# Kernel tuning notes

Measured on AMD Instinct MI355X. Metric: run time of the kernel, lower is better.

Reference implementation:

```python
import jax, jax.numpy as jnp
import numpy as np

HIDDEN = 2560
HEADS = 32
HEAD_DIM = HIDDEN // HEADS  # 80
ROT = HEAD_DIM // 2         # partial_rotary_factor=0.5 -> 40
B = 2
S = 2048
T = B * S
THETA = 10000.0


def setup_inputs() -> dict:
    key = jax.random.key(0)
    k0, k1, k2, k3, k4 = jax.random.split(key, 5)
    hidden_states = jax.random.normal(k0, (T, HIDDEN), jnp.float32)
    w_qkv = jax.random.normal(k1, (3 * HIDDEN, HIDDEN), jnp.float32) * 0.02
    b_qkv = jax.random.normal(k2, (3 * HIDDEN,), jnp.float32) * 0.02
    w_o = jax.random.normal(k3, (HIDDEN, HIDDEN), jnp.float32) * 0.02
    b_o = jax.random.normal(k4, (HIDDEN,), jnp.float32) * 0.02
    # rotary tables for positions 0..S-1 per sequence, rotary_dim=ROT
    pos = jnp.tile(jnp.arange(S, dtype=jnp.float32), B)  # [T]
    inv_freq = 1.0 / (THETA ** (jnp.arange(0, ROT, 2, dtype=jnp.float32) / ROT))  # [ROT//2]
    freqs = pos[:, None] * inv_freq[None, :]  # [T, ROT//2]
    return {
        "hidden_states": hidden_states,
        "w_qkv": w_qkv,
        "b_qkv": b_qkv,
        "w_o": w_o,
        "b_o": b_o,
        "cos": jnp.cos(freqs),
        "sin": jnp.sin(freqs),
        "batch": B,
    }


def _apply_rope(x, cos, sin):
    # x: [T, H, D]; rotate first ROT dims NeoX-style (rotate_half)
    half = ROT // 2
    x1 = x[..., :half]
    x2 = x[..., half:ROT]
    c = cos[:, None, :]
    s = sin[:, None, :]
    return jnp.concatenate([x1 * c - x2 * s, x1 * s + x2 * c, x[..., ROT:]], axis=-1)


def reference(hidden_states, w_qkv, b_qkv, w_o, b_o, cos, sin, batch):
    t, hdim = hidden_states.shape
    seq = t // batch
    # fused QKV projection (with bias)
    qkv = hidden_states @ w_qkv.T + b_qkv  # [T, 3*HIDDEN]
    q, k, v = jnp.split(qkv, 3, axis=1)
    q = _apply_rope(q.reshape(t, HEADS, HEAD_DIM), cos, sin)
    k = _apply_rope(k.reshape(t, HEADS, HEAD_DIM), cos, sin)
    v = v.reshape(t, HEADS, HEAD_DIM)
    # prefill causal attention per sequence
    qb = q.reshape(batch, seq, HEADS, HEAD_DIM)
    kb = k.reshape(batch, seq, HEADS, HEAD_DIM)
    vb = v.reshape(batch, seq, HEADS, HEAD_DIM)
    scale = 1.0 / jnp.sqrt(jnp.float32(HEAD_DIM))
    scores = jnp.einsum("bqhd,bkhd->bhqk", qb, kb) * scale  # [B,H,S,S]
    causal = jnp.tril(jnp.ones((seq, seq), dtype=bool))
    scores = jnp.where(causal[None, None], scores, jnp.finfo(scores.dtype).min)
    attn = jax.nn.softmax(scores, axis=-1)
    out = jnp.einsum("bhqk,bkhd->bqhd", attn, vb).reshape(t, HIDDEN)
    return out @ w_o.T + b_o
```

## Files before the change

### kernel.cpp

```cpp
#include <hip/hip_runtime.h>
#include <hip/hip_bf16.h>

#define HID   2560
#define NH    32
#define HD    80
#define SEQ   2048
#define TTOT  4096
#define QKVN  7680

typedef float  f32x4  __attribute__((ext_vector_type(4)));
typedef short  short8 __attribute__((ext_vector_type(8)));
typedef __bf16 bf16x8 __attribute__((ext_vector_type(8)));
typedef __hip_bfloat16 bf16;

__device__ __forceinline__ float bf2f(bf16 h) { return __bfloat162float(h); }
__device__ __forceinline__ bf16  f2bf(float f) { return __float2bfloat16(f); }

__device__ __forceinline__ f32x4 mfma16(short8 a, short8 b, f32x4 c) {
  return __builtin_amdgcn_mfma_f32_16x16x32_bf16(
      __builtin_bit_cast(bf16x8, a), __builtin_bit_cast(bf16x8, b), c, 0, 0, 0);
}

typedef __attribute__((address_space(1))) const unsigned int as1_uint;
typedef __attribute__((address_space(3))) unsigned int       as3_uint;
__device__ __forceinline__ void gld16(const void* g, void* l) {
  __builtin_amdgcn_global_load_lds((as1_uint*)g, (as3_uint*)l, 16, 0, 0);
}

__global__ void detect_kernel(const unsigned short* __restrict__ hid, int* flag) {
  const int tid = threadIdx.x;
  const unsigned short u = hid[2 * (tid * 997)];
  const int e = (u >> 7) & 0xFF;
  const int sane = (u == 0 || (e >= 0x60 && e <= 0x8A)) ? 1 : 0;
  __shared__ int cnt;
  if (tid == 0) cnt = 0;
  __syncthreads();
  atomicAdd(&cnt, sane);
  __syncthreads();
  if (tid == 0) *flag = (cnt < 160) ? 1 : 0;
}

__global__ void convert_kernel(const void* __restrict__ src, bf16* __restrict__ dst,
                               int n8, const int* __restrict__ flag) {
  const bool isf32 = (*flag != 0);
  for (int i = blockIdx.x * 256 + threadIdx.x; i < n8; i += gridDim.x * 256) {
    if (isf32) {
      const float4* s = (const float4*)src;
      float4 a = s[2 * i], b = s[2 * i + 1];
      __align__(16) bf16 o8[8] = {f2bf(a.x), f2bf(a.y), f2bf(a.z), f2bf(a.w),
                                  f2bf(b.x), f2bf(b.y), f2bf(b.z), f2bf(b.w)};
      *(uint4*)(dst + 8 * i) = *(const uint4*)o8;
    } else {
      *(uint4*)(dst + 8 * i) = ((const uint4*)src)[i];
    }
  }
}

__global__ void emit_kernel(const bf16* __restrict__ src, void* __restrict__ dst,
                            int n8, const int* __restrict__ flag) {
  const bool isf32 = (*flag != 0);
  for (int i = blockIdx.x * 256 + threadIdx.x; i < n8; i += gridDim.x * 256) {
    uint4 v = *(const uint4*)(src + 8 * i);
    if (isf32) {
      const bf16* b = (const bf16*)&v;
      float4* d = (float4*)dst;
      d[2 * i]     = make_float4(bf2f(b[0]), bf2f(b[1]), bf2f(b[2]), bf2f(b[3]));
      d[2 * i + 1] = make_float4(bf2f(b[4]), bf2f(b[5]), bf2f(b[6]), bf2f(b[7]));
    } else {
      ((uint4*)dst)[i] = v;
    }
  }
}

__global__ __launch_bounds__(512, 2) void gemm256_bias(
    const bf16* __restrict__ A, const bf16* __restrict__ B,
    const bf16* __restrict__ bias, bf16* __restrict__ C,
    int M, int N, int K)
{
  __shared__ __align__(16) bf16 lA[3][16384];
  __shared__ __align__(16) bf16 lB[2][16384];

  const int tid  = threadIdx.x;
  const int wid  = tid >> 6;
  const int lane = tid & 63;
  const int quad = lane >> 4;
  const int l15  = lane & 15;
  const int wr   = wid >> 2;
  const int wc   = wid & 3;

  int wgid;
  {
    const int nwg = gridDim.x;
    const int q = nwg >> 3, r = nwg & 7;
    const int xcd = blockIdx.x & 7, lin = blockIdx.x >> 3;
    wgid = (xcd < r ? xcd * (q + 1) : r * (q + 1) + (xcd - r) * q) + lin;
  }
  const int gx = M >> 8;
  const int m0 = (wgid % gx) << 8;
  const int n0 = (wgid / gx) << 8;

  const int NT = K >> 6;

  const int rr   = tid >> 3;
  const int cbyt = ((tid & 7) << 4) ^ ((rr & 7) << 4);
  const size_t o1 = (size_t)rr * K + (cbyt >> 1);
  const size_t o2 = o1 + (size_t)64 * K;

  const bf16* Ab = A + (size_t)m0 * K;
  const bf16* Bb = B + (size_t)n0 * K;

#define STAGEA(bufsel, half, tt)                                               \
  {                                                                            \
    const bf16* _s = Ab + (size_t)(half) * 128 * K + (size_t)(tt) * 64;        \
    bf16* _d = &lA[bufsel][(half) * 8192 + wid * 512];                         \
    gld16(_s + o1, _d);                                                        \
    gld16(_s + o2, _d + 4096);                                                 \
  }
#define STAGEB(bufsel, half, tt)                                               \
  {                                                                            \
    const bf16* _s = Bb + (size_t)(half) * 128 * K + (size_t)(tt) * 64;        \
    bf16* _d = &lB[bufsel][(half) * 8192 + wid * 512];                         \
    gld16(_s + o1, _d);                                                        \
    gld16(_s + o2, _d + 4096);                                                 \
  }

#define WAIT_LGKM0                                                             \
  do {                                                                         \
    asm volatile("s_waitcnt lgkmcnt(0)" ::: "memory");                         \
    __builtin_amdgcn_sched_barrier(0);                                         \
  } while (0)
#define WAIT_VM(n) asm volatile("s_waitcnt vmcnt(" #n ")" ::: "memory")

  const int csw0 = ((quad ^ (l15 & 7)) << 4);
  const int csw1 = (((4 | quad) ^ (l15 & 7)) << 4);

  f32x4 acc[8][4];
#pragma unroll
  for (int i = 0; i < 8; ++i)
#pragma unroll
    for (int j = 0; j < 4; ++j) acc[i][j] = (f32x4)0.f;

  short8 a[4][2], b23[2][2], b01A[2][2], b01B[2][2];

  STAGEA(0, 0, 0); STAGEA(0, 1, 0);
  STAGEB(0, 0, 0); STAGEB(0, 1, 0);
  if (NT > 1) {
    STAGEA(1, 0, 1); STAGEA(1, 1, 1);
    STAGEB(1, 0, 1); STAGEB(1, 1, 1);
    WAIT_VM(8);
  } else {
    WAIT_VM(0);
  }
  __builtin_amdgcn_s_barrier();
#pragma unroll
  for (int n = 0; n < 2; ++n) {
    const char* p = (const char*)lB[0] + (size_t)(wc * 64 + n * 16 + l15) * 128;
    b01A[n][0] = *(const short8*)(p + csw0);
    b01A[n][1] = *(const short8*)(p + csw1);
  }

#define KTILE(T, B01U, B01L)                                                   \
  do {                                                                         \
    const int _t = (T);                                                        \
    const bf16* Al = lA[_t % 3];                                               \
    const bf16* Bl = lB[_t & 1];                                               \
    const bf16* Bln = lB[(_t + 1) & 1];                                        \
    const bool stg = (_t + 2 < NT);                                            \
    const bool nxt = (_t + 1 < NT);                                            \
             \
    _Pragma("unroll") for (int mi = 0; mi < 4; ++mi) {                         \
      const char* p = (const char*)Al + (size_t)(wr * 128 + mi * 16 + l15) * 128; \
      a[mi][0] = *(const short8*)(p + csw0);                                   \
      a[mi][1] = *(const short8*)(p + csw1);                                   \
    }                                                                          \
    if (stg) STAGEA((_t + 2) % 3, 0, _t + 2);                                  \
    WAIT_LGKM0;                                                                \
    __builtin_amdgcn_s_setprio(1);                                             \
    _Pragma("unroll") for (int mi = 0; mi < 4; ++mi)                           \
      _Pragma("unroll") for (int n = 0; n < 2; ++n) {                          \
        acc[mi][n] = mfma16(a[mi][0], B01U[n][0], acc[mi][n]);                 \
        acc[mi][n] = mfma16(a[mi][1], B01U[n][1], acc[mi][n]);                 \
      }                                                                        \
    __builtin_amdgcn_s_setprio(0);                                             \
                \
    _Pragma("unroll") for (int n = 0; n < 2; ++n) {                            \
      const char* p = (const char*)Bl + (size_t)(wc * 64 + (2 + n) * 16 + l15) * 128; \
      b23[n][0] = *(const short8*)(p + csw0);                                  \
      b23[n][1] = *(const short8*)(p + csw1);                                  \
    }                                                                          \
    if (stg) STAGEA((_t + 2) % 3, 1, _t + 2);                                  \
    WAIT_LGKM0;                                                                \
    __builtin_amdgcn_s_setprio(1);                                             \
    _Pragma("unroll") for (int mi = 0; mi < 4; ++mi)                           \
      _Pragma("unroll") for (int n = 0; n < 2; ++n) {                          \
        acc[mi][2 + n] = mfma16(a[mi][0], b23[n][0], acc[mi][2 + n]);          \
        acc[mi][2 + n] = mfma16(a[mi][1], b23[n][1], acc[mi][2 + n]);          \
      }                                                                        \
    __builtin_amdgcn_s_setprio(0);                                             \
                                               \
    _Pragma("unroll") for (int mi = 0; mi < 4; ++mi) {                         \
      const char* p = (const char*)Al + (size_t)(wr * 128 + 64 + mi * 16 + l15) * 128; \
      a[mi][0] = *(const short8*)(p + csw0);                                   \
      a[mi][1] = *(const short8*)(p + csw1);                                   \
    }                                                                          \
    if (stg) STAGEB(_t & 1, 0, _t + 2);                                        \
    if (stg) { WAIT_VM(6); } else { WAIT_VM(0); }                              \
    __builtin_amdgcn_s_barrier();                                              \
    WAIT_LGKM0;                                                                \
    __builtin_amdgcn_s_setprio(1);                                             \
    _Pragma("unroll") for (int mi = 0; mi < 4; ++mi)                           \
      _Pragma("unroll") for (int n = 0; n < 2; ++n) {                          \
        acc[4 + mi][2 + n] = mfma16(a[mi][0], b23[n][0], acc[4 + mi][2 + n]);  \
        acc[4 + mi][2 + n] = mfma16(a[mi][1], b23[n][1], acc[4 + mi][2 + n]);  \
      }                                                                        \
    __builtin_amdgcn_s_setprio(0);                                             \
          \
    if (nxt) {                                                                 \
      _Pragma("unroll") for (int n = 0; n < 2; ++n) {                          \
        const char* p = (const char*)Bln + (size_t)(wc * 64 + n * 16 + l15) * 128; \
        B01L[n][0] = *(const short8*)(p + csw0);                               \
        B01L[n][1] = *(const short8*)(p + csw1);                               \
      }                                                                        \
    }                                                                          \
    if (stg) STAGEB(_t & 1, 1, _t + 2);                                        \
    __builtin_amdgcn_s_setprio(1);                                             \
    _Pragma("unroll") for (int mi = 0; mi < 4; ++mi)                           \
      _Pragma("unroll") for (int n = 0; n < 2; ++n) {                          \
        acc[4 + mi][n] = mfma16(a[mi][0], B01U[n][0], acc[4 + mi][n]);         \
        acc[4 + mi][n] = mfma16(a[mi][1], B01U[n][1], acc[4 + mi][n]);         \
      }                                                                        \
    __builtin_amdgcn_s_setprio(0);                                             \
    __builtin_amdgcn_s_barrier();                                              \
  } while (0)

  for (int t = 0; t < NT; t += 2) {
    KTILE(t, b01A, b01B);
    if (t + 1 < NT) KTILE(t + 1, b01B, b01A);
  }
#undef KTILE
#undef STAGEA
#undef STAGEB
#undef WAIT_LGKM0
#undef WAIT_VM

  const int crow = m0 + wr * 128 + quad * 4;
  const int ccol = n0 + wc * 64 + l15;
#pragma unroll
  for (int n = 0; n < 4; ++n) {
    const float bv = bf2f(bias[ccol + n * 16]);
#pragma unroll
    for (int mi = 0; mi < 8; ++mi) {
      const int rb = crow + mi * 16;
#pragma unroll
      for (int r = 0; r < 4; ++r)
        C[(size_t)(rb + r) * N + ccol + n * 16] = f2bf(acc[mi][n][r] + bv);
    }
  }
}

__global__ __launch_bounds__(256) void rope_kernel(
    const bf16* __restrict__ qkv, const bf16* __restrict__ cosb,
    const bf16* __restrict__ sinb, bf16* __restrict__ Qr, bf16* __restrict__ Kr)
{
  const int t = blockIdx.x;
  const int b = t >> 11;
  const int s = t & 2047;
  const float qscale = 0.11180339887498949f;

  __shared__ float cs[20], sn[20];
  if (threadIdx.x < 20) cs[threadIdx.x] = bf2f(cosb[t * 20 + threadIdx.x]);
  if (threadIdx.x >= 32 && threadIdx.x < 52)
    sn[threadIdx.x - 32] = bf2f(sinb[t * 20 + (threadIdx.x - 32)]);
  __syncthreads();

  const bf16* qrow = qkv + (size_t)t * QKVN;
  const bf16* krow = qrow + HID;

  for (int idx = threadIdx.x; idx < HID; idx += 256) {
    const int h = idx / HD, d = idx % HD;
    const size_t off = ((size_t)(b * NH + h) * SEQ + s) * HD + d;
    float q, k;
    if (d < 20) {
      q = bf2f(qrow[h * HD + d]) * cs[d] - bf2f(qrow[h * HD + d + 20]) * sn[d];
      k = bf2f(krow[h * HD + d]) * cs[d] - bf2f(krow[h * HD + d + 20]) * sn[d];
    } else if (d < 40) {
      q = bf2f(qrow[h * HD + d - 20]) * sn[d - 20] + bf2f(qrow[h * HD + d]) * cs[d - 20];
      k = bf2f(krow[h * HD + d - 20]) * sn[d - 20] + bf2f(krow[h * HD + d]) * cs[d - 20];
    } else {
      q = bf2f(qrow[h * HD + d]);
      k = bf2f(krow[h * HD + d]);
    }
    Qr[off] = f2bf(q * qscale);
    Kr[off] = f2bf(k);
  }
}

__global__ __launch_bounds__(256) void vtrans_kernel(
    const bf16* __restrict__ qkv, bf16* __restrict__ Vt)
{
  const int bh = blockIdx.x;
  const int s0 = blockIdx.y * 64;
  const int b = bh >> 5, h = bh & 31;
  __shared__ bf16 tile[64][81];

  for (int e = threadIdx.x; e < 64 * HD; e += 256) {
    const int r = e / HD, d = e % HD;
    tile[r][d] = qkv[(size_t)(b * SEQ + s0 + r) * QKVN + 2 * HID + h * HD + d];
  }
  __syncthreads();
  for (int e = threadIdx.x; e < 64 * HD; e += 256) {
    const int d = e >> 6, r = e & 63;
    Vt[((size_t)bh * HD + d) * SEQ + s0 + r] = tile[r][d];
  }
}

__global__ __launch_bounds__(256, 3) void attn_kernel(
    const bf16* __restrict__ Qr, const bf16* __restrict__ Kr,
    const bf16* __restrict__ Vt, bf16* __restrict__ O)
{
  const int raw  = blockIdx.x;
  const int slot = raw >> 3;
  const int qblk = 15 - (slot & 15);
  const int bh   = ((slot >> 4) << 3) + (raw & 7);

  const int tid  = threadIdx.x;
  const int wave = tid >> 6;
  const int lane = tid & 63;
  const int quad = lane >> 4;
  const int l15  = lane & 15;
  const int qbase = qblk * 128;

  __shared__ __align__(16) bf16 stage[12544];
  __shared__ __align__(16) bf16 pt[4 * 2 * 1152];

  bf16* kt = stage;
  bf16* vt = stage + 5632;

  if (tid < 144) {
    const unsigned one2 = 0x3F803F80u;
    *(uint4*)&vt[5760 + tid * 8] = (uint4){one2, one2, one2, one2};
  }

  int goff[6];
#pragma unroll
  for (int it = 0; it < 6; it++) {
    const int j = tid + it * 256;
    if (j < 704) {
      const int r = j / 11; int c = j - 11 * r; if (c > 9) c = 0;
      goff[it] = r * 160 + c * 16;
    } else {
      const int j2 = j - 704;
      const int r = j2 / 9; int c = j2 - 9 * r; if (c > 7) c = 0;
      goff[it] = r * 4096 + c * 16;
    }
  }

  short8 aq[2][3];
#pragma unroll
  for (int f = 0; f < 2; f++) {
    const bf16* Qb = Qr + ((size_t)bh * SEQ + qbase + f * 64 + wave * 16 + l15) * HD + quad * 8;
    aq[f][0] = *(const short8*)(Qb);
    aq[f][1] = *(const short8*)(Qb + 32);
    aq[f][2] = *(const short8*)(Qb + 64);
    if (quad >= 2) aq[f][2] = (short8)0;
  }

  f32x4 o[2][6];
#pragma unroll
  for (int f = 0; f < 2; f++)
    for (int nt = 0; nt < 6; nt++) o[f][nt] = (f32x4)0.f;
  float m_i[2] = {-3e38f, -3e38f};

  const char* Kb8 = (const char*)(Kr + (size_t)bh * SEQ * HD);
  const char* Vb8 = (const char*)(Vt + (size_t)bh * HD * SEQ);
  const int nsteps = 2 * qblk + 2;
  const int rmax0 = qbase + wave * 16 + 15;

  for (int step = 0; step < nsteps; step++) {
    const int kvo = step * 64;
    const bool act0 = (kvo <= rmax0);

    __syncthreads();
    {
      const char* kb = Kb8 + kvo * 160;
      const char* vb = Vb8 + kvo * 2;
#pragma unroll
      for (int it = 0; it < 6; it++) {
        const int j = tid + it * 256;
        if (j < 1424) {
          bf16* ldsb = stage + (it * 256 + wave * 64) * 8;
          gld16((j < 704) ? (kb + goff[it]) : (vb + goff[it]), ldsb);
        }
      }
    }
    __syncthreads();

    f32x4 sv[2][4];
#pragma unroll
    for (int nt = 0; nt < 4; nt++) {
      const bf16* kr = &kt[(nt * 16 + l15) * 88 + quad * 8];
      short8 b0 = *(const short8*)(kr);
      short8 b1 = *(const short8*)(kr + 32);
      short8 b2 = *(const short8*)(kr + 64);
      if (act0) {
        f32x4 s = mfma16(b0, aq[0][0], (f32x4)0.f);
        s = mfma16(b1, aq[0][1], s);
        sv[0][nt] = mfma16(b2, aq[0][2], s);
      }
      f32x4 s1 = mfma16(b0, aq[1][0], (f32x4)0.f);
      s1 = mfma16(b1, aq[1][1], s1);
      sv[1][nt] = mfma16(b2, aq[1][2], s1);
    }

#pragma unroll
    for (int f = 0; f < 2; f++) {
      if (f == 0 && !act0) continue;
      const int mrel = qbase + f * 64 + wave * 16 - kvo;
      if (mrel < 63) {
        const int qrel = mrel + l15;
#pragma unroll
        for (int nt = 0; nt < 4; nt++) {
          f32x4 t = sv[f][nt];
#pragma unroll
          for (int r = 0; r < 4; r++)
            t[r] = (nt * 16 + quad * 4 + r <= qrel) ? t[r] : -3e38f;
          sv[f][nt] = t;
        }
      }
      float mx = fmaxf(fmaxf(sv[f][0][0], sv[f][0][1]), fmaxf(sv[f][0][2], sv[f][0][3]));
#pragma unroll
      for (int nt = 1; nt < 4; nt++)
        mx = fmaxf(mx, fmaxf(fmaxf(sv[f][nt][0], sv[f][nt][1]),
                             fmaxf(sv[f][nt][2], sv[f][nt][3])));
      mx = fmaxf(mx, __shfl_xor(mx, 16, 64));
      mx = fmaxf(mx, __shfl_xor(mx, 32, 64));
      const float mnew = fmaxf(m_i[f], mx);
      const float alpha = __expf(m_i[f] - mnew);
      m_i[f] = mnew;

      bf16* ptw = pt + (wave * 2 + f) * 1152;
#pragma unroll
      for (int nt = 0; nt < 4; nt++) {
        __align__(8) bf16 p4[4];
#pragma unroll
        for (int r = 0; r < 4; r++) p4[r] = f2bf(__expf(sv[f][nt][r] - mnew));
        *(unsigned long long*)&ptw[l15 * 72 + nt * 16 + quad * 4] =
            *(const unsigned long long*)p4;
      }
      float av[4];
#pragma unroll
      for (int r = 0; r < 4; r++) av[r] = __shfl(alpha, quad * 4 + r, 64);
#pragma unroll
      for (int nt = 0; nt < 6; nt++) {
        f32x4 t = o[f][nt];
        t[0] *= av[0]; t[1] *= av[1]; t[2] *= av[2]; t[3] *= av[3];
        o[f][nt] = t;
      }
    }

    asm volatile("s_waitcnt lgkmcnt(0)" ::: "memory");
    short8 pa00 = (short8)0, pa01 = (short8)0, pa10, pa11;
    {
      const bf16* p0 = pt + (wave * 2 + 0) * 1152 + l15 * 72 + quad * 8;
      const bf16* p1 = pt + (wave * 2 + 1) * 1152 + l15 * 72 + quad * 8;
      if (act0) { pa00 = *(const short8*)p0; pa01 = *(const short8*)(p0 + 32); }
      pa10 = *(const short8*)p1; pa11 = *(const short8*)(p1 + 32);
    }
#pragma unroll
    for (int nt = 0; nt < 6; nt++) {
      const bf16* vr = &vt[(nt * 16 + l15) * 72 + quad * 8];
      short8 v0 = *(const short8*)(vr);
      short8 v1 = *(const short8*)(vr + 32);
      if (act0) {
        o[0][nt] = mfma16(pa00, v0, o[0][nt]);
        o[0][nt] = mfma16(pa01, v1, o[0][nt]);
      }
      o[1][nt] = mfma16(pa10, v0, o[1][nt]);
      o[1][nt] = mfma16(pa11, v1, o[1][nt]);
    }
  }

  const int b = bh >> 5, h = bh & 31;
#pragma unroll
  for (int f = 0; f < 2; f++)
#pragma unroll
    for (int r = 0; r < 4; r++) {
      const float inv = 1.0f / o[f][5][r];
      const int trow = b * SEQ + qbase + f * 64 + wave * 16 + quad * 4 + r;
#pragma unroll
      for (int nt = 0; nt < 5; nt++)
        O[(size_t)trow * HID + h * HD + nt * 16 + l15] = f2bf(o[f][nt][r] * inv);
    }
}

extern "C" void kernel_launch(void* const* d_in, const int* in_sizes, int n_in,
                              void* d_out, int out_size, void* d_ws, size_t ws_size,
                              hipStream_t stream) {
  (void)in_sizes; (void)n_in; (void)ws_size;
  char* wsb = (char*)d_ws;

  int*  flag   = (int*) (wsb + 0);
  bf16* cos_c  = (bf16*)(wsb + 1024);
  bf16* sin_c  = (bf16*)(wsb + 165888);
  bf16* bqkv_c = (bf16*)(wsb + 329728);
  bf16* bo_c   = (bf16*)(wsb + 345088);
  bf16* wo_c   = (bf16*)(wsb + 1048576);
  bf16* qkv    = (bf16*)(wsb + 14155776);
  bf16* hid_c  = (bf16*)(wsb + 77070336);
  bf16* wqkv_c = (bf16*)(wsb + 98041856);
  bf16* Qr     = (bf16*)(wsb + 77070336);
  bf16* Kr     = (bf16*)(wsb + 98041856);
  bf16* Vt     = (bf16*)(wsb + 119013376);
  bf16* attn   = (bf16*)(wsb + 14155776);
  bf16* obuf   = (bf16*)(wsb + 35127296);

  detect_kernel<<<1, 256, 0, stream>>>((const unsigned short*)d_in[0], flag);
  convert_kernel<<<1024, 256, 0, stream>>>(d_in[0], hid_c,  TTOT * HID / 8, flag);
  convert_kernel<<<1024, 256, 0, stream>>>(d_in[1], wqkv_c, QKVN * HID / 8, flag);
  convert_kernel<<<4,    256, 0, stream>>>(d_in[2], bqkv_c, QKVN / 8,       flag);
  convert_kernel<<<1024, 256, 0, stream>>>(d_in[3], wo_c,   HID * HID / 8,  flag);
  convert_kernel<<<2,    256, 0, stream>>>(d_in[4], bo_c,   HID / 8,        flag);
  convert_kernel<<<40,   256, 0, stream>>>(d_in[5], cos_c,  TTOT * 20 / 8,  flag);
  convert_kernel<<<40,   256, 0, stream>>>(d_in[6], sin_c,  TTOT * 20 / 8,  flag);

  gemm256_bias<<<dim3((TTOT / 256) * (QKVN / 256)), 512, 0, stream>>>(
      hid_c, wqkv_c, bqkv_c, qkv, TTOT, QKVN, HID);
  rope_kernel<<<dim3(TTOT), 256, 0, stream>>>(qkv, cos_c, sin_c, Qr, Kr);
  vtrans_kernel<<<dim3(64, SEQ / 64), 256, 0, stream>>>(qkv, Vt);
  attn_kernel<<<dim3(1024), 256, 0, stream>>>(Qr, Kr, Vt, attn);
  gemm256_bias<<<dim3((TTOT / 256) * (HID / 256)), 512, 0, stream>>>(
      attn, wo_c, bo_c, obuf, TTOT, HID, HID);
  emit_kernel<<<1024, 256, 0, stream>>>(obuf, d_out, out_size / 8, flag);
}
```

Before: 591.7 us.

## Rebalance GEMM k-loop sync into two phases and vectorize rope kernel

The GEMM inner k-tile loop is restructured from four waits and barriers per tile into two phases. Each phase issues the LDS fragment reads and the global-to-LDS stages together, then waits once, and the setprio hints are dropped. Separately, the rope kernel now has each thread handle four contiguous elements with 8-byte vector loads and stores, using 320 threads per block instead of scalar per-element work. The GEMM change aims to cut barrier and waitcnt stalls but may weaken latency hiding between the LDS reads and the MFMAs.

```diff
diff --git a/kernel.cpp b/kernel.cpp
--- a/kernel.cpp
+++ b/kernel.cpp
@@ -10,11 +10,16 @@
 
 typedef float  f32x4  __attribute__((ext_vector_type(4)));
 typedef short  short8 __attribute__((ext_vector_type(8)));
+typedef unsigned short us4 __attribute__((ext_vector_type(4)));
 typedef __bf16 bf16x8 __attribute__((ext_vector_type(8)));
 typedef __hip_bfloat16 bf16;
 
 __device__ __forceinline__ float bf2f(bf16 h) { return __bfloat162float(h); }
 __device__ __forceinline__ bf16  f2bf(float f) { return __float2bfloat16(f); }
+__device__ __forceinline__ float us2f(unsigned short u) {
+  unsigned int x = ((unsigned int)u) << 16;
+  return __builtin_bit_cast(float, x);
+}
 
 __device__ __forceinline__ f32x4 mfma16(short8 a, short8 b, f32x4 c) {
   return __builtin_amdgcn_mfma_f32_16x16x32_bf16(
@@ -124,13 +129,6 @@
     gld16(_s + o2, _d + 4096);                                                 \
   }
 
-#define WAIT_LGKM0                                                             \
-  do {                                                                         \
-    asm volatile("s_waitcnt lgkmcnt(0)" ::: "memory");                         \
-    __builtin_amdgcn_sched_barrier(0);                                         \
-  } while (0)
-#define WAIT_VM(n) asm volatile("s_waitcnt vmcnt(" #n ")" ::: "memory")
-
   const int csw0 = ((quad ^ (l15 & 7)) << 4);
   const int csw1 = (((4 | quad) ^ (l15 & 7)) << 4);
 
@@ -147,9 +145,9 @@
   if (NT > 1) {
     STAGEA(1, 0, 1); STAGEA(1, 1, 1);
     STAGEB(1, 0, 1); STAGEB(1, 1, 1);
-    WAIT_VM(8);
+    asm volatile("s_waitcnt vmcnt(8)" ::: "memory");
   } else {
-    WAIT_VM(0);
+    asm volatile("s_waitcnt vmcnt(0)" ::: "memory");
   }
   __builtin_amdgcn_s_barrier();
 #pragma unroll
@@ -167,54 +165,39 @@
     const bf16* Bln = lB[(_t + 1) & 1];                                        \
     const bool stg = (_t + 2 < NT);                                            \
     const bool nxt = (_t + 1 < NT);                                            \
-             \
+        \
     _Pragma("unroll") for (int mi = 0; mi < 4; ++mi) {                         \
       const char* p = (const char*)Al + (size_t)(wr * 128 + mi * 16 + l15) * 128; \
       a[mi][0] = *(const short8*)(p + csw0);                                   \
       a[mi][1] = *(const short8*)(p + csw1);                                   \
     }                                                                          \
-    if (stg) STAGEA((_t + 2) % 3, 0, _t + 2);                                  \
-    WAIT_LGKM0;                                                                \
-    __builtin_amdgcn_s_setprio(1);                                             \
+    _Pragma("unroll") for (int n = 0; n < 2; ++n) {                            \
+      const char* p = (const char*)Bl + (size_t)(wc * 64 + (2 + n) * 16 + l15) * 128; \
+      b23[n][0] = *(const short8*)(p + csw0);                                  \
+      b23[n][1] = *(const short8*)(p + csw1);                                  \
+    }                                                                          \
+    if (stg) { STAGEA((_t + 2) % 3, 0, _t + 2); STAGEA((_t + 2) % 3, 1, _t + 2); } \
     _Pragma("unroll") for (int mi = 0; mi < 4; ++mi)                           \
       _Pragma("unroll") for (int n = 0; n < 2; ++n) {                          \
         acc[mi][n] = mfma16(a[mi][0], B01U[n][0], acc[mi][n]);                 \
         acc[mi][n] = mfma16(a[mi][1], B01U[n][1], acc[mi][n]);                 \
       }                                                                        \
-    __builtin_amdgcn_s_setprio(0);                                             \
-                \
-    _Pragma("unroll") for (int n = 0; n < 2; ++n) {                            \
-      const char* p = (const char*)Bl + (size_t)(wc * 64 + (2 + n) * 16 + l15) * 128; \
-      b23[n][0] = *(const short8*)(p + csw0);                                  \
-      b23[n][1] = *(const short8*)(p + csw1);                                  \
-    }                                                                          \
-    if (stg) STAGEA((_t + 2) % 3, 1, _t + 2);                                  \
-    WAIT_LGKM0;                                                                \
-    __builtin_amdgcn_s_setprio(1);                                             \
     _Pragma("unroll") for (int mi = 0; mi < 4; ++mi)                           \
       _Pragma("unroll") for (int n = 0; n < 2; ++n) {                          \
         acc[mi][2 + n] = mfma16(a[mi][0], b23[n][0], acc[mi][2 + n]);          \
         acc[mi][2 + n] = mfma16(a[mi][1], b23[n][1], acc[mi][2 + n]);          \
       }                                                                        \
-    __builtin_amdgcn_s_setprio(0);                                             \
-                                               \
+        \
+    asm volatile("s_waitcnt lgkmcnt(0)" ::: "memory");                         \
+    if (stg) { asm volatile("s_waitcnt vmcnt(4)" ::: "memory"); }              \
+    else     { asm volatile("s_waitcnt vmcnt(0)" ::: "memory"); }              \
+    __builtin_amdgcn_s_barrier();                                              \
+                                                            \
     _Pragma("unroll") for (int mi = 0; mi < 4; ++mi) {                         \
       const char* p = (const char*)Al + (size_t)(wr * 128 + 64 + mi * 16 + l15) * 128; \
       a[mi][0] = *(const short8*)(p + csw0);                                   \
       a[mi][1] = *(const short8*)(p + csw1);                                   \
     }                                                                          \
-    if (stg) STAGEB(_t & 1, 0, _t + 2);                                        \
-    if (stg) { WAIT_VM(6); } else { WAIT_VM(0); }                              \
-    __builtin_amdgcn_s_barrier();                                              \
-    WAIT_LGKM0;                                                                \
-    __builtin_amdgcn_s_setprio(1);                                             \
-    _Pragma("unroll") for (int mi = 0; mi < 4; ++mi)                           \
-      _Pragma("unroll") for (int n = 0; n < 2; ++n) {                          \
-        acc[4 + mi][2 + n] = mfma16(a[mi][0], b23[n][0], acc[4 + mi][2 + n]);  \
-        acc[4 + mi][2 + n] = mfma16(a[mi][1], b23[n][1], acc[4 + mi][2 + n]);  \
-      }                                                                        \
-    __builtin_amdgcn_s_setprio(0);                                             \
-          \
     if (nxt) {                                                                 \
       _Pragma("unroll") for (int n = 0; n < 2; ++n) {                          \
         const char* p = (const char*)Bln + (size_t)(wc * 64 + n * 16 + l15) * 128; \
@@ -222,14 +205,19 @@
         B01L[n][1] = *(const short8*)(p + csw1);                               \
       }                                                                        \
     }                                                                          \
-    if (stg) STAGEB(_t & 1, 1, _t + 2);                                        \
-    __builtin_amdgcn_s_setprio(1);                                             \
+    if (stg) { STAGEB(_t & 1, 0, _t + 2); STAGEB(_t & 1, 1, _t + 2); }         \
+    _Pragma("unroll") for (int mi = 0; mi < 4; ++mi)                           \
+      _Pragma("unroll") for (int n = 0; n < 2; ++n) {                          \
+        acc[4 + mi][2 + n] = mfma16(a[mi][0], b23[n][0], acc[4 + mi][2 + n]);  \
+        acc[4 + mi][2 + n] = mfma16(a[mi][1], b23[n][1], acc[4 + mi][2 + n]);  \
+      }                                                                        \
     _Pragma("unroll") for (int mi = 0; mi < 4; ++mi)                           \
       _Pragma("unroll") for (int n = 0; n < 2; ++n) {                          \
         acc[4 + mi][n] = mfma16(a[mi][0], B01U[n][0], acc[4 + mi][n]);         \
         acc[4 + mi][n] = mfma16(a[mi][1], B01U[n][1], acc[4 + mi][n]);         \
       }                                                                        \
-    __builtin_amdgcn_s_setprio(0);                                             \
+               \
+    asm volatile("s_waitcnt lgkmcnt(0)" ::: "memory");                         \
     __builtin_amdgcn_s_barrier();                                              \
   } while (0)
 
@@ -240,8 +228,6 @@
 #undef KTILE
 #undef STAGEA
 #undef STAGEB
-#undef WAIT_LGKM0
-#undef WAIT_VM
 
   const int crow = m0 + wr * 128 + quad * 4;
   const int ccol = n0 + wc * 64 + l15;
@@ -258,7 +244,7 @@
   }
 }
 
-__global__ __launch_bounds__(256) void rope_kernel(
+__global__ __launch_bounds__(320) void rope_kernel(
     const bf16* __restrict__ qkv, const bf16* __restrict__ cosb,
     const bf16* __restrict__ sinb, bf16* __restrict__ Qr, bf16* __restrict__ Kr)
 {
@@ -269,29 +255,52 @@
 
   __shared__ float cs[20], sn[20];
   if (threadIdx.x < 20) cs[threadIdx.x] = bf2f(cosb[t * 20 + threadIdx.x]);
-  if (threadIdx.x >= 32 && threadIdx.x < 52)
-    sn[threadIdx.x - 32] = bf2f(sinb[t * 20 + (threadIdx.x - 32)]);
+  if (threadIdx.x >= 64 && threadIdx.x < 84)
+    sn[threadIdx.x - 64] = bf2f(sinb[t * 20 + (threadIdx.x - 64)]);
   __syncthreads();
 
   const bf16* qrow = qkv + (size_t)t * QKVN;
   const bf16* krow = qrow + HID;
 
-  for (int idx = threadIdx.x; idx < HID; idx += 256) {
-    const int h = idx / HD, d = idx % HD;
-    const size_t off = ((size_t)(b * NH + h) * SEQ + s) * HD + d;
-    float q, k;
-    if (d < 20) {
-      q = bf2f(qrow[h * HD + d]) * cs[d] - bf2f(qrow[h * HD + d + 20]) * sn[d];
-      k = bf2f(krow[h * HD + d]) * cs[d] - bf2f(krow[h * HD + d + 20]) * sn[d];
-    } else if (d < 40) {
-      q = bf2f(qrow[h * HD + d - 20]) * sn[d - 20] + bf2f(qrow[h * HD + d]) * cs[d - 20];
-      k = bf2f(krow[h * HD + d - 20]) * sn[d - 20] + bf2f(krow[h * HD + d]) * cs[d - 20];
+#pragma unroll
+  for (int it = 0; it < 2; ++it) {
+    const int ci = threadIdx.x + it * 320;
+    const int h = ci / 20, c = ci % 20;
+    const int d0 = c * 4;
+    const bf16* qp = qrow + h * HD + d0;
+    const bf16* kp = krow + h * HD + d0;
+    const us4 qv = *(const us4*)qp;
+    const us4 kv = *(const us4*)kp;
+    float qo[4], ko[4];
+    if (c < 5) {
+      const us4 q2 = *(const us4*)(qp + 20);
+      const us4 k2 = *(const us4*)(kp + 20);
+#pragma unroll
+      for (int j = 0; j < 4; ++j) {
+        qo[j] = us2f(qv[j]) * cs[d0 + j] - us2f(q2[j]) * sn[d0 + j];
+        ko[j] = us2f(kv[j]) * cs[d0 + j] - us2f(k2[j]) * sn[d0 + j];
+      }
+    } else if (c < 10) {
+      const us4 q1 = *(const us4*)(qp - 20);
+      const us4 k1 = *(const us4*)(kp - 20);
+#pragma unroll
+      for (int j = 0; j < 4; ++j) {
+        qo[j] = us2f(q1[j]) * sn[d0 - 20 + j] + us2f(qv[j]) * cs[d0 - 20 + j];
+        ko[j] = us2f(k1[j]) * sn[d0 - 20 + j] + us2f(kv[j]) * cs[d0 - 20 + j];
+      }
     } else {
-      q = bf2f(qrow[h * HD + d]);
-      k = bf2f(krow[h * HD + d]);
-    }
-    Qr[off] = f2bf(q * qscale);
-    Kr[off] = f2bf(k);
+#pragma unroll
+      for (int j = 0; j < 4; ++j) { qo[j] = us2f(qv[j]); ko[j] = us2f(kv[j]); }
+    }
+    const size_t off = ((size_t)(b * NH + h) * SEQ + s) * HD + d0;
+    __align__(8) bf16 oq[4], ok[4];
+#pragma unroll
+    for (int j = 0; j < 4; ++j) {
+      oq[j] = f2bf(qo[j] * qscale);
+      ok[j] = f2bf(ko[j]);
+    }
+    *(unsigned long long*)(Qr + off) = *(const unsigned long long*)oq;
+    *(unsigned long long*)(Kr + off) = *(const unsigned long long*)ok;
   }
 }
 
@@ -525,7 +534,7 @@
 
   gemm256_bias<<<dim3((TTOT / 256) * (QKVN / 256)), 512, 0, stream>>>(
       hid_c, wqkv_c, bqkv_c, qkv, TTOT, QKVN, HID);
-  rope_kernel<<<dim3(TTOT), 256, 0, stream>>>(qkv, cos_c, sin_c, Qr, Kr);
+  rope_kernel<<<dim3(TTOT), 320, 0, stream>>>(qkv, cos_c, sin_c, Qr, Kr);
   vtrans_kernel<<<dim3(64, SEQ / 64), 256, 0, stream>>>(qkv, Vt);
   attn_kernel<<<dim3(1024), 256, 0, stream>>>(Qr, Kr, Vt, attn);
   gemm256_bias<<<dim3((TTOT / 256) * (HID / 256)), 512, 0, stream>>>(
```

After: 554.4 us. 1.07x faster.
